# Kernel optimization log

Measured on AMD Instinct MI355X. Metric: run time of the kernel, lower is better.

Reference implementation:

```python
import jax, jax.numpy as jnp
import numpy as np

UP_RATIO = 2
DOWN_RATIO = 2
KS = 12  # up/down FIR kernel size
EPS = 1e-9


def kaiser_sinc_filter1d(cutoff, half_width, kernel_size):
    even = kernel_size % 2 == 0
    half_size = kernel_size // 2
    delta_f = 4.0 * half_width
    A = 2.285 * (half_size - 1) * np.pi * delta_f + 7.95
    if A > 50.0:
        beta = 0.1102 * (A - 8.7)
    elif A >= 21.0:
        beta = 0.5842 * (A - 21.0) ** 0.4 + 0.07886 * (A - 21.0)
    else:
        beta = 0.0
    window = np.kaiser(kernel_size, beta)
    if even:
        time = np.arange(-half_size, half_size) + 0.5
    else:
        time = np.arange(kernel_size) - half_size
    f = 2.0 * cutoff * window * np.sinc(2.0 * cutoff * time)
    f = f / f.sum()
    return f.astype(np.float32)


FILT_UP = jnp.asarray(kaiser_sinc_filter1d(0.5 / UP_RATIO, 0.6 / UP_RATIO, KS))
FILT_DOWN = jnp.asarray(kaiser_sinc_filter1d(0.5 / DOWN_RATIO, 0.6 / DOWN_RATIO, KS))


def _depthwise(x, w, strides, padding, lhs_dilation):
    # x: [B, C, T]; run depthwise FIR by folding channels into batch.
    B, C, T = x.shape
    y = jax.lax.conv_general_dilated(
        x.reshape(B * C, 1, T), w.reshape(1, 1, -1),
        window_strides=(strides,), padding=padding,
        lhs_dilation=(lhs_dilation,),
        dimension_numbers=("NCH", "OIH", "NCH"))
    return y.reshape(B, C, -1)


def upsample(x):
    # zero-stuff by ratio + symmetric kaiser-sinc FIR (== conv_transpose1d)
    k, r = KS, UP_RATIO
    pad = k // r - 1
    pad_left = pad * r + (k - r) // 2
    pad_right = pad * r + (k - r + 1) // 2
    x = jnp.pad(x, ((0, 0), (0, 0), (pad, pad)), mode="edge")
    y = r * _depthwise(x, FILT_UP, 1, [(k - 1, k - 1)], r)
    return y[..., pad_left:-pad_right]  # [B, C, 2T]


def downsample(x):
    k, r = KS, DOWN_RATIO
    pad_left = k // 2 - 1  # even kernel
    pad_right = k // 2
    x = jnp.pad(x, ((0, 0), (0, 0), (pad_left, pad_right)), mode="edge")
    return _depthwise(x, FILT_DOWN, r, "VALID", 1)  # [B, C, T]


def snake_beta(x, alpha_log, beta_log):
    # x + 1/(beta+eps) * sin(alpha*x)^2, alpha/beta = exp(log params), per channel
    a = jnp.exp(alpha_log)[None, :, None]
    b = jnp.exp(beta_log)[None, :, None]
    return x + (1.0 / (b + EPS)) * jnp.square(jnp.sin(a * x))


def alias_free_act(x, alpha_log, beta_log):
    return downsample(snake_beta(upsample(x), alpha_log, beta_log))


def conv1d(x, w, b, pad, dilation=1):
    y = jax.lax.conv_general_dilated(
        x, w, (1,), [(pad, pad)], rhs_dilation=(dilation,),
        dimension_numbers=("NCH", "OIH", "NCH"))
    return y + b[None, :, None]


def setup_inputs() -> dict:
    key = jax.random.key(0)
    ks = jax.random.split(key, 3)
    B, C, T = 8, 512, 8192
    x = jax.random.normal(ks[0], (B, C, T), dtype=jnp.float32)
    # init_weights: normal(0, 0.01)
    w1 = 0.01 * jax.random.normal(ks[1], (C, C, 3), dtype=jnp.float32)
    w2 = 0.01 * jax.random.normal(ks[2], (C, C, 3), dtype=jnp.float32)
    b1 = jnp.zeros((C,), dtype=jnp.float32)
    b2 = jnp.zeros((C,), dtype=jnp.float32)
    # SnakeBeta alpha_logscale=True: log-params init to zeros (alpha=beta=1)
    alpha1 = jnp.zeros((C,), dtype=jnp.float32)
    beta1 = jnp.zeros((C,), dtype=jnp.float32)
    alpha2 = jnp.zeros((C,), dtype=jnp.float32)
    beta2 = jnp.zeros((C,), dtype=jnp.float32)
    return {"x": x, "w1": w1, "b1": b1, "w2": w2, "b2": b2,
            "alpha1": alpha1, "beta1": beta1, "alpha2": alpha2, "beta2": beta2}


def reference(x, w1, b1, w2, b2, alpha1, beta1, alpha2, beta2):
    # AMPBlock0.forward: xt = a2(c2(a1(c1(a1(x))))); x = xt + x
    xt = alias_free_act(x, alpha1, beta1)
    xt = conv1d(xt, w1, b1, pad=1, dilation=1)  # dilation[0] == 1
    xt = alias_free_act(xt, alpha1, beta1)
    xt = conv1d(xt, w2, b2, pad=1, dilation=1)
    xt = alias_free_act(xt, alpha2, beta2)
    return xt + x
```

## Files before the change

kernel.cpp:

```cpp
#include <hip/hip_runtime.h>
#include <hip/hip_bf16.h>
#include <math.h>

#ifndef M_PI
#define M_PI 3.14159265358979323846
#endif

typedef __attribute__((ext_vector_type(8))) short bf16x8;
typedef __attribute__((ext_vector_type(4))) float f32x4;

struct Filt { float f[12]; };

static double bessel_i0(double x) {
  double sum = 1.0, term = 1.0;
  for (int k = 1; k < 64; ++k) {
    term *= x / (2.0 * k);
    double t2 = term * term;
    sum += t2;
    if (t2 < 1e-22 * sum) break;
  }
  return sum;
}

static void compute_filter(float* out12) {
  const int ks = 12;
  const double cutoff = 0.25, half_width = 0.3;
  const int half_size = 6;
  double delta_f = 4.0 * half_width;
  double A = 2.285 * (half_size - 1) * M_PI * delta_f + 7.95;
  double beta;
  if (A > 50.0)       beta = 0.1102 * (A - 8.7);
  else if (A >= 21.0) beta = 0.5842 * pow(A - 21.0, 0.4) + 0.07886 * (A - 21.0);
  else                beta = 0.0;
  double i0b = bessel_i0(beta);
  double f[12], s = 0.0;
  for (int n = 0; n < ks; ++n) {
    double ratio = (n - (ks - 1) / 2.0) / ((ks - 1) / 2.0);
    double arg = 1.0 - ratio * ratio;
    double wnd = bessel_i0(beta * sqrt(arg > 0.0 ? arg : 0.0)) / i0b;
    double time = (n - half_size) + 0.5;
    double xx = 2.0 * cutoff * time;
    double sinc = (xx == 0.0) ? 1.0 : sin(M_PI * xx) / (M_PI * xx);
    f[n] = 2.0 * cutoff * wnd * sinc;
    s += f[n];
  }
  for (int n = 0; n < ks; ++n) out12[n] = (float)(f[n] / s);
}

__device__ __forceinline__ ushort f2bf(float f) {
  __hip_bfloat16 h = __float2bfloat16(f);
  return *(ushort*)&h;
}

__device__ __forceinline__ void gl_lds16(const void* g, void* l) {
  __builtin_amdgcn_global_load_lds(
      (const __attribute__((address_space(1))) unsigned int*)g,
      (__attribute__((address_space(3))) unsigned int*)l, 16, 0, 0);
}

template <typename TIN, bool TOUT>
__global__ __launch_bounds__(512, 4) void act2(
    const TIN* __restrict__ in, void* __restrict__ out_,
    const float* __restrict__ alpha_log, const float* __restrict__ beta_log,
    const float* __restrict__ resid, int C, int T, Filt fl)
{
  __shared__ float xs[64 * 75];
  __shared__ float ys[TOUT ? 1 : 64 * 65];
  const int t0 = blockIdx.x * 64;
  const int c0 = blockIdx.y * 64;
  const int b  = blockIdx.z;
  const int tid = threadIdx.x;

  constexpr int NSTG = 64 * 74;
  float tmp[10];
#pragma unroll
  for (int k = 0; k < 10; ++k) {
    int i = tid + k * 512;
    if (i < NSTG) {
      int c = i / 74, j = i - c * 74;
      int t = min(max(t0 - 5 + j, 0), T - 1);
      tmp[k] = (float)in[((long)(b * C + c0 + c)) * T + t];
    }
  }
#pragma unroll
  for (int k = 0; k < 10; ++k) {
    int i = tid + k * 512;
    if (i < NSTG) {
      int c = i / 74, j = i - c * 74;
      xs[c * 75 + j] = tmp[k];
    }
  }
  __syncthreads();

  const int c  = tid & 63;
  const int tg = tid >> 6;
  const int tb = t0 + tg * 8;
  const float a  = __expf(alpha_log[c0 + c]);
  const float rb = 1.0f / (__expf(beta_log[c0 + c]) + 1e-9f);

  float sbv[26];
  const bool interior = (tb >= 8) && (tb <= T - 16);
  if (interior) {
    float xv[18];
    const float* xr = xs + c * 75 + tg * 8;
#pragma unroll
    for (int m = 0; m < 18; ++m) xv[m] = xr[m];
#pragma unroll
    for (int m = 0; m <= 12; ++m) {
      float uo = fl.f[1] * xv[m]     + fl.f[3] * xv[m + 1] + fl.f[5]  * xv[m + 2]
               + fl.f[7] * xv[m + 3] + fl.f[9] * xv[m + 4] + fl.f[11] * xv[m + 5];
      float ue = fl.f[0] * xv[m]     + fl.f[2] * xv[m + 1] + fl.f[4]  * xv[m + 2]
               + fl.f[6] * xv[m + 3] + fl.f[8] * xv[m + 4] + fl.f[10] * xv[m + 5];
      uo *= 2.0f; ue *= 2.0f;
      float s0 = __sinf(a * uo);
      float s1 = __sinf(a * ue);
      sbv[2 * m]     = uo + rb * s0 * s0;
      sbv[2 * m + 1] = ue + rb * s1 * s1;
    }
  } else {
    const float* xr = xs + c * 75;
#pragma unroll
    for (int j = 0; j < 26; ++j) {
      int p = 2 * tb - 5 + j;
      int pc = min(max(p, 0), 2 * T - 1);
      float up;
      if (pc & 1) {
        int q = (pc - 1) >> 1;
        int base = q - t0 + 3;
        up = fl.f[1] * xr[base]     + fl.f[3] * xr[base + 1] + fl.f[5]  * xr[base + 2]
           + fl.f[7] * xr[base + 3] + fl.f[9] * xr[base + 4] + fl.f[11] * xr[base + 5];
      } else {
        int q = pc >> 1;
        int base = q - t0 + 2;
        up = fl.f[0] * xr[base]     + fl.f[2] * xr[base + 1] + fl.f[4]  * xr[base + 2]
           + fl.f[6] * xr[base + 3] + fl.f[8] * xr[base + 4] + fl.f[10] * xr[base + 5];
      }
      up *= 2.0f;
      float s = __sinf(a * up);
      sbv[j] = up + rb * s * s;
    }
  }

  float acc[8];
#pragma unroll
  for (int i = 0; i < 8; ++i) {
    float s = 0.0f;
#pragma unroll
    for (int u = 0; u < 12; ++u) s += fl.f[u] * sbv[2 * i + u];
    acc[i] = s;
  }

  if constexpr (TOUT) {
    __hip_bfloat16* out = (__hip_bfloat16*)out_;
#pragma unroll
    for (int i = 0; i < 8; ++i)
      out[((long)b * T + tb + i) * C + c0 + c] = __float2bfloat16(acc[i]);
  } else {
    float* out = (float*)out_;
    const int cc0 = tid >> 4,        tq0 = (tid & 15) * 4;
    const int cc1 = cc0 + 32,        tq1 = tq0;
    const long o0 = ((long)(b * C + c0 + cc0)) * T + t0 + tq0;
    const long o1 = ((long)(b * C + c0 + cc1)) * T + t0 + tq1;
    const float4 r0 = *(const float4*)(resid + o0);
    const float4 r1 = *(const float4*)(resid + o1);
#pragma unroll
    for (int i = 0; i < 8; ++i) ys[c * 65 + tg * 8 + i] = acc[i];
    __syncthreads();
    float4 v0, v1;
    v0.x = ys[cc0 * 65 + tq0]     + r0.x;
    v0.y = ys[cc0 * 65 + tq0 + 1] + r0.y;
    v0.z = ys[cc0 * 65 + tq0 + 2] + r0.z;
    v0.w = ys[cc0 * 65 + tq0 + 3] + r0.w;
    v1.x = ys[cc1 * 65 + tq1]     + r1.x;
    v1.y = ys[cc1 * 65 + tq1 + 1] + r1.y;
    v1.z = ys[cc1 * 65 + tq1 + 2] + r1.z;
    v1.w = ys[cc1 * 65 + tq1 + 3] + r1.w;
    *(float4*)(out + o0) = v0;
    *(float4*)(out + o1) = v1;
  }
}

__global__ __launch_bounds__(256) void wconv(
    const float* __restrict__ w, ushort* __restrict__ wbf, int C)
{
  int idx = blockIdx.x * 256 + threadIdx.x;
  int total = 3 * C * C;
  if (idx >= total) return;
  int d = idx / (C * C);
  int r = idx - d * C * C;
  wbf[idx] = f2bf(w[(long)r * 3 + d]);
}

#define MT 64
#define NTC 256
#define BK 32

__global__ __launch_bounds__(256) void conv_mfma(
    const __hip_bfloat16* __restrict__ inT,
    const ushort* __restrict__ wbf,
    const float* __restrict__ bias,
    __hip_bfloat16* __restrict__ out,
    int C, int T)
{
  __shared__ ushort wl[3][MT][BK];
  __shared__ ushort xs[NTC + 2][BK];
  const int t0  = blockIdx.x * NTC;
  const int co0 = blockIdx.y * MT;
  const int b   = blockIdx.z;
  const int tid  = threadIdx.x;
  const int lane = tid & 63;
  const int wave = tid >> 6;
  const int ln15 = lane & 15;
  const int quad = lane >> 4;
  const ushort* inU = (const ushort*)inT;

  f32x4 acc[4][4];
#pragma unroll
  for (int mi = 0; mi < 4; ++mi)
#pragma unroll
    for (int ni = 0; ni < 4; ++ni) acc[mi][ni] = (f32x4){0.f, 0.f, 0.f, 0.f};

  ushort* wlf = &wl[0][0][0];
  ushort* xsf = &xs[0][0];

  for (int ci0 = 0; ci0 < C; ci0 += BK) {
    __syncthreads();
#pragma unroll
    for (int it = 0; it < 3; ++it) {
      int g = it * 256 + tid;
      int d = g >> 8, co = (g >> 2) & 63, seg = g & 3;
      const ushort* gsrc = wbf + ((long)d * C + co0 + co) * C + ci0 + seg * 8;
      gl_lds16(gsrc, wlf + (size_t)(it * 256 + (tid & ~63)) * 8);
    }
#pragma unroll
    for (int it = 0; it < 4; ++it) {
      int g = it * 256 + tid + 4;
      int tl = g >> 2, seg = g & 3;
      int t = t0 - 1 + tl;
      const ushort* gsrc = inU + ((long)b * T + t) * C + ci0 + seg * 8;
      gl_lds16(gsrc, xsf + (size_t)(it * 256 + (tid & ~63) + 4) * 8);
    }
    if (tid < 8) {
      int g = (tid < 4) ? tid : (1028 + tid - 4);
      int tl = g >> 2, seg = g & 3;
      int t = t0 - 1 + tl;
      uint4 v = {0u, 0u, 0u, 0u};
      if (t >= 0 && t < T)
        v = *(const uint4*)(inU + ((long)b * T + t) * C + ci0 + seg * 8);
      *(uint4*)&xs[tl][seg * 8] = v;
    }
    __syncthreads();

#pragma unroll
    for (int d = 0; d < 3; ++d) {
      bf16x8 afr[4], bfr[4];
#pragma unroll
      for (int mi = 0; mi < 4; ++mi)
        afr[mi] = *(const bf16x8*)&wl[d][mi * 16 + ln15][quad * 8];
#pragma unroll
      for (int ni = 0; ni < 4; ++ni)
        bfr[ni] = *(const bf16x8*)&xs[wave * 64 + ni * 16 + ln15 + d][quad * 8];
#pragma unroll
      for (int mi = 0; mi < 4; ++mi)
#pragma unroll
        for (int ni = 0; ni < 4; ++ni)
          acc[mi][ni] = __builtin_amdgcn_mfma_f32_16x16x32_bf16(
              afr[mi], bfr[ni], acc[mi][ni], 0, 0, 0);
    }
  }

#pragma unroll
  for (int mi = 0; mi < 4; ++mi) {
#pragma unroll
    for (int r = 0; r < 4; ++r) {
      int co = co0 + mi * 16 + quad * 4 + r;
      float bv = bias[co];
      long orow = ((long)(b * C + co)) * T;
#pragma unroll
      for (int ni = 0; ni < 4; ++ni) {
        int t = t0 + wave * 64 + ni * 16 + ln15;
        out[orow + t] = __float2bfloat16(acc[mi][ni][r] + bv);
      }
    }
  }
}

extern "C" void kernel_launch(void* const* d_in, const int* in_sizes, int n_in,
                              void* d_out, int out_size, void* d_ws, size_t ws_size,
                              hipStream_t stream) {
  const float* x      = (const float*)d_in[0];
  const float* w1     = (const float*)d_in[1];
  const float* b1     = (const float*)d_in[2];
  const float* w2     = (const float*)d_in[3];
  const float* b2     = (const float*)d_in[4];
  const float* alpha1 = (const float*)d_in[5];
  const float* beta1  = (const float*)d_in[6];
  const float* alpha2 = (const float*)d_in[7];
  const float* beta2  = (const float*)d_in[8];
  float* out = (float*)d_out;

  const int C = in_sizes[2];
  const long total = (long)in_sizes[0];
  const int T = 8192;
  const int B = (int)(total / ((long)C * T));

  __hip_bfloat16* ws0 = (__hip_bfloat16*)d_ws;
  __hip_bfloat16* ws1 = ws0 + (size_t)B * C * T;
  ushort* w1bf = (ushort*)d_out;
  ushort* w2bf = w1bf + (size_t)3 * C * C;

  Filt fl;
  compute_filter(fl.f);

  dim3 actGrid(T / 64, C / 64, B);
  dim3 convGrid(T / NTC, C / MT, B);
  int wblocks = (3 * C * C + 255) / 256;

  wconv<<<wblocks, 256, 0, stream>>>(w1, w1bf, C);
  wconv<<<wblocks, 256, 0, stream>>>(w2, w2bf, C);
  act2<float, true><<<actGrid, 512, 0, stream>>>(x, ws0, alpha1, beta1, nullptr, C, T, fl);
  conv_mfma<<<convGrid, 256, 0, stream>>>(ws0, w1bf, b1, ws1, C, T);
  act2<__hip_bfloat16, true><<<actGrid, 512, 0, stream>>>(ws1, ws0, alpha1, beta1, nullptr, C, T, fl);
  conv_mfma<<<convGrid, 256, 0, stream>>>(ws0, w2bf, b2, ws1, C, T);
  act2<__hip_bfloat16, false><<<actGrid, 512, 0, stream>>>(ws1, out, alpha2, beta2, x, C, T, fl);
}
```

Before: 892.2 us.

## Make act2 blocks loop over eight time tiles with register-prefetched inputs

Each activation block now walks eight consecutive 64-sample time tiles instead of one. While the current tile is being computed, the next tile's input is prefetched into registers, so global load latency can overlap with the sin/FIR arithmetic. The grid shrinks eightfold, which lowers parallelism per launch (B*C/64*16 blocks) and adds an extra barrier per tile plus higher register pressure from the double-buffered temporaries.

Measured after the change: 1.237 ms. +38.6%, slower.

```diff
diff --git a/kernel.cpp b/kernel.cpp
--- a/kernel.cpp
+++ b/kernel.cpp
@@ -58,6 +58,29 @@
       (__attribute__((address_space(3))) unsigned int*)l, 16, 0, 0);
 }
 
+#define NSTG (64 * 74)
+
+#define PREFETCH(T0, TMP)                                                \
+  _Pragma("unroll")                                                      \
+  for (int k = 0; k < 10; ++k) {                                         \
+    int i = tid + k * 512;                                               \
+    if (i < NSTG) {                                                      \
+      int cI = i / 74, jI = i - cI * 74;                                 \
+      int t = min(max((T0) - 5 + jI, 0), T - 1);                         \
+      TMP[k] = (float)in[((long)(b * C + c0 + cI)) * T + t];             \
+    }                                                                    \
+  }
+
+#define WRITE_XS(TMP)                                                    \
+  _Pragma("unroll")                                                      \
+  for (int k = 0; k < 10; ++k) {                                         \
+    int i = tid + k * 512;                                               \
+    if (i < NSTG) {                                                      \
+      int cI = i / 74, jI = i - cI * 74;                                 \
+      xs[cI * 75 + jI] = TMP[k];                                         \
+    }                                                                    \
+  }
+
 template <typename TIN, bool TOUT>
 __global__ __launch_bounds__(512, 4) void act2(
     const TIN* __restrict__ in, void* __restrict__ out_,
@@ -66,117 +89,112 @@
 {
   __shared__ float xs[64 * 75];
   __shared__ float ys[TOUT ? 1 : 64 * 65];
-  const int t0 = blockIdx.x * 64;
+  const int NT = 8;
+  const int tbase = blockIdx.x * (64 * NT);
   const int c0 = blockIdx.y * 64;
   const int b  = blockIdx.z;
   const int tid = threadIdx.x;
 
-  constexpr int NSTG = 64 * 74;
-  float tmp[10];
-#pragma unroll
-  for (int k = 0; k < 10; ++k) {
-    int i = tid + k * 512;
-    if (i < NSTG) {
-      int c = i / 74, j = i - c * 74;
-      int t = min(max(t0 - 5 + j, 0), T - 1);
-      tmp[k] = (float)in[((long)(b * C + c0 + c)) * T + t];
-    }
-  }
-#pragma unroll
-  for (int k = 0; k < 10; ++k) {
-    int i = tid + k * 512;
-    if (i < NSTG) {
-      int c = i / 74, j = i - c * 74;
-      xs[c * 75 + j] = tmp[k];
-    }
-  }
-  __syncthreads();
-
   const int c  = tid & 63;
   const int tg = tid >> 6;
-  const int tb = t0 + tg * 8;
   const float a  = __expf(alpha_log[c0 + c]);
   const float rb = 1.0f / (__expf(beta_log[c0 + c]) + 1e-9f);
 
-  float sbv[26];
-  const bool interior = (tb >= 8) && (tb <= T - 16);
-  if (interior) {
-    float xv[18];
-    const float* xr = xs + c * 75 + tg * 8;
-#pragma unroll
-    for (int m = 0; m < 18; ++m) xv[m] = xr[m];
-#pragma unroll
-    for (int m = 0; m <= 12; ++m) {
-      float uo = fl.f[1] * xv[m]     + fl.f[3] * xv[m + 1] + fl.f[5]  * xv[m + 2]
-               + fl.f[7] * xv[m + 3] + fl.f[9] * xv[m + 4] + fl.f[11] * xv[m + 5];
-      float ue = fl.f[0] * xv[m]     + fl.f[2] * xv[m + 1] + fl.f[4]  * xv[m + 2]
-               + fl.f[6] * xv[m + 3] + fl.f[8] * xv[m + 4] + fl.f[10] * xv[m + 5];
-      uo *= 2.0f; ue *= 2.0f;
-      float s0 = __sinf(a * uo);
-      float s1 = __sinf(a * ue);
-      sbv[2 * m]     = uo + rb * s0 * s0;
-      sbv[2 * m + 1] = ue + rb * s1 * s1;
-    }
-  } else {
-    const float* xr = xs + c * 75;
-#pragma unroll
-    for (int j = 0; j < 26; ++j) {
-      int p = 2 * tb - 5 + j;
-      int pc = min(max(p, 0), 2 * T - 1);
-      float up;
-      if (pc & 1) {
-        int q = (pc - 1) >> 1;
-        int base = q - t0 + 3;
-        up = fl.f[1] * xr[base]     + fl.f[3] * xr[base + 1] + fl.f[5]  * xr[base + 2]
-           + fl.f[7] * xr[base + 3] + fl.f[9] * xr[base + 4] + fl.f[11] * xr[base + 5];
-      } else {
-        int q = pc >> 1;
-        int base = q - t0 + 2;
-        up = fl.f[0] * xr[base]     + fl.f[2] * xr[base + 1] + fl.f[4]  * xr[base + 2]
-           + fl.f[6] * xr[base + 3] + fl.f[8] * xr[base + 4] + fl.f[10] * xr[base + 5];
+  float tmpA[10], tmpB[10];
+  PREFETCH(tbase, tmpA);
+
+  for (int tt = 0; tt < NT; ++tt) {
+    const int t0 = tbase + tt * 64;
+    WRITE_XS(tmpA);
+    __syncthreads();
+    if (tt + 1 < NT) { PREFETCH(t0 + 64, tmpB); }
+
+    const int tb = t0 + tg * 8;
+    float sbv[26];
+    const bool interior = (tb >= 8) && (tb <= T - 16);
+    if (interior) {
+      float xv[18];
+      const float* xr = xs + c * 75 + tg * 8;
+#pragma unroll
+      for (int m = 0; m < 18; ++m) xv[m] = xr[m];
+#pragma unroll
+      for (int m = 0; m <= 12; ++m) {
+        float uo = fl.f[1] * xv[m]     + fl.f[3] * xv[m + 1] + fl.f[5]  * xv[m + 2]
+                 + fl.f[7] * xv[m + 3] + fl.f[9] * xv[m + 4] + fl.f[11] * xv[m + 5];
+        float ue = fl.f[0] * xv[m]     + fl.f[2] * xv[m + 1] + fl.f[4]  * xv[m + 2]
+                 + fl.f[6] * xv[m + 3] + fl.f[8] * xv[m + 4] + fl.f[10] * xv[m + 5];
+        uo *= 2.0f; ue *= 2.0f;
+        float s0 = __sinf(a * uo);
+        float s1 = __sinf(a * ue);
+        sbv[2 * m]     = uo + rb * s0 * s0;
+        sbv[2 * m + 1] = ue + rb * s1 * s1;
       }
-      up *= 2.0f;
-      float s = __sinf(a * up);
-      sbv[j] = up + rb * s * s;
-    }
-  }
-
-  float acc[8];
-#pragma unroll
-  for (int i = 0; i < 8; ++i) {
-    float s = 0.0f;
-#pragma unroll
-    for (int u = 0; u < 12; ++u) s += fl.f[u] * sbv[2 * i + u];
-    acc[i] = s;
-  }
-
-  if constexpr (TOUT) {
-    __hip_bfloat16* out = (__hip_bfloat16*)out_;
-#pragma unroll
-    for (int i = 0; i < 8; ++i)
-      out[((long)b * T + tb + i) * C + c0 + c] = __float2bfloat16(acc[i]);
-  } else {
-    float* out = (float*)out_;
-    const int cc0 = tid >> 4,        tq0 = (tid & 15) * 4;
-    const int cc1 = cc0 + 32,        tq1 = tq0;
-    const long o0 = ((long)(b * C + c0 + cc0)) * T + t0 + tq0;
-    const long o1 = ((long)(b * C + c0 + cc1)) * T + t0 + tq1;
-    const float4 r0 = *(const float4*)(resid + o0);
-    const float4 r1 = *(const float4*)(resid + o1);
-#pragma unroll
-    for (int i = 0; i < 8; ++i) ys[c * 65 + tg * 8 + i] = acc[i];
-    __syncthreads();
-    float4 v0, v1;
-    v0.x = ys[cc0 * 65 + tq0]     + r0.x;
-    v0.y = ys[cc0 * 65 + tq0 + 1] + r0.y;
-    v0.z = ys[cc0 * 65 + tq0 + 2] + r0.z;
-    v0.w = ys[cc0 * 65 + tq0 + 3] + r0.w;
-    v1.x = ys[cc1 * 65 + tq1]     + r1.x;
-    v1.y = ys[cc1 * 65 + tq1 + 1] + r1.y;
-    v1.z = ys[cc1 * 65 + tq1 + 2] + r1.z;
-    v1.w = ys[cc1 * 65 + tq1 + 3] + r1.w;
-    *(float4*)(out + o0) = v0;
-    *(float4*)(out + o1) = v1;
+    } else {
+      const float* xr = xs + c * 75;
+#pragma unroll
+      for (int j = 0; j < 26; ++j) {
+        int p = 2 * tb - 5 + j;
+        int pc = min(max(p, 0), 2 * T - 1);
+        float up;
+        if (pc & 1) {
+          int q = (pc - 1) >> 1;
+          int base = q - t0 + 3;
+          up = fl.f[1] * xr[base]     + fl.f[3] * xr[base + 1] + fl.f[5]  * xr[base + 2]
+             + fl.f[7] * xr[base + 3] + fl.f[9] * xr[base + 4] + fl.f[11] * xr[base + 5];
+        } else {
+          int q = pc >> 1;
+          int base = q - t0 + 2;
+          up = fl.f[0] * xr[base]     + fl.f[2] * xr[base + 1] + fl.f[4]  * xr[base + 2]
+             + fl.f[6] * xr[base + 3] + fl.f[8] * xr[base + 4] + fl.f[10] * xr[base + 5];
+        }
+        up *= 2.0f;
+        float s = __sinf(a * up);
+        sbv[j] = up + rb * s * s;
+      }
+    }
+
+    float acc[8];
+#pragma unroll
+    for (int i = 0; i < 8; ++i) {
+      float s = 0.0f;
+#pragma unroll
+      for (int u = 0; u < 12; ++u) s += fl.f[u] * sbv[2 * i + u];
+      acc[i] = s;
+    }
+
+    if constexpr (TOUT) {
+      __hip_bfloat16* out = (__hip_bfloat16*)out_;
+#pragma unroll
+      for (int i = 0; i < 8; ++i)
+        out[((long)b * T + tb + i) * C + c0 + c] = __float2bfloat16(acc[i]);
+      __syncthreads();
+    } else {
+      float* out = (float*)out_;
+      const int cc0 = tid >> 4,   tq0 = (tid & 15) * 4;
+      const int cc1 = cc0 + 32,   tq1 = tq0;
+      const long o0 = ((long)(b * C + c0 + cc0)) * T + t0 + tq0;
+      const long o1 = ((long)(b * C + c0 + cc1)) * T + t0 + tq1;
+      const float4 r0 = *(const float4*)(resid + o0);
+      const float4 r1 = *(const float4*)(resid + o1);
+#pragma unroll
+      for (int i = 0; i < 8; ++i) ys[c * 65 + tg * 8 + i] = acc[i];
+      __syncthreads();
+      float4 v0, v1;
+      v0.x = ys[cc0 * 65 + tq0]     + r0.x;
+      v0.y = ys[cc0 * 65 + tq0 + 1] + r0.y;
+      v0.z = ys[cc0 * 65 + tq0 + 2] + r0.z;
+      v0.w = ys[cc0 * 65 + tq0 + 3] + r0.w;
+      v1.x = ys[cc1 * 65 + tq1]     + r1.x;
+      v1.y = ys[cc1 * 65 + tq1 + 1] + r1.y;
+      v1.z = ys[cc1 * 65 + tq1 + 2] + r1.z;
+      v1.w = ys[cc1 * 65 + tq1 + 3] + r1.w;
+      *(float4*)(out + o0) = v0;
+      *(float4*)(out + o1) = v1;
+      __syncthreads();
+    }
+
+#pragma unroll
+    for (int k = 0; k < 10; ++k) tmpA[k] = tmpB[k];
   }
 }
 
@@ -312,7 +330,7 @@
   Filt fl;
   compute_filter(fl.f);
 
-  dim3 actGrid(T / 64, C / 64, B);
+  dim3 actGrid(T / 512, C / 64, B);
   dim3 convGrid(T / NTC, C / MT, B);
   int wblocks = (3 * C * C + 255) / 256;
 
```

## Loop act2 over channel tiles with register-prefetched vectorized loads

Applied to the files above, without the earlier changes.

The activation kernel now gives each block all channels for one time tile and loops over 64-channel chunks. The next chunk's input is prefetched into registers with 16-byte vector loads while the current chunk is computed, replacing the earlier scalar strided loads. This is meant to hide global load latency and cut per-load instruction overhead. The cost is a grid that shrinks by a factor of C/64, which lowers parallelism, plus extra registers and barriers per iteration.

Result: faster. 770.0 us (-13.7%).

```diff
diff --git a/kernel.cpp b/kernel.cpp
--- a/kernel.cpp
+++ b/kernel.cpp
@@ -64,119 +64,189 @@
     const float* __restrict__ alpha_log, const float* __restrict__ beta_log,
     const float* __restrict__ resid, int C, int T, Filt fl)
 {
-  __shared__ float xs[64 * 75];
+  __shared__ float xs[64 * 81];
   __shared__ float ys[TOUT ? 1 : 64 * 65];
   const int t0 = blockIdx.x * 64;
-  const int c0 = blockIdx.y * 64;
   const int b  = blockIdx.z;
   const int tid = threadIdx.x;
-
-  constexpr int NSTG = 64 * 74;
-  float tmp[10];
-#pragma unroll
-  for (int k = 0; k < 10; ++k) {
-    int i = tid + k * 512;
-    if (i < NSTG) {
-      int c = i / 74, j = i - c * 74;
-      int t = min(max(t0 - 5 + j, 0), T - 1);
-      tmp[k] = (float)in[((long)(b * C + c0 + c)) * T + t];
-    }
-  }
-#pragma unroll
-  for (int k = 0; k < 10; ++k) {
-    int i = tid + k * 512;
-    if (i < NSTG) {
-      int c = i / 74, j = i - c * 74;
-      xs[c * 75 + j] = tmp[k];
-    }
-  }
-  __syncthreads();
-
   const int c  = tid & 63;
   const int tg = tid >> 6;
-  const int tb = t0 + tg * 8;
-  const float a  = __expf(alpha_log[c0 + c]);
-  const float rb = 1.0f / (__expf(beta_log[c0 + c]) + 1e-9f);
-
-  float sbv[26];
-  const bool interior = (tb >= 8) && (tb <= T - 16);
-  if (interior) {
-    float xv[18];
-    const float* xr = xs + c * 75 + tg * 8;
-#pragma unroll
-    for (int m = 0; m < 18; ++m) xv[m] = xr[m];
-#pragma unroll
-    for (int m = 0; m <= 12; ++m) {
-      float uo = fl.f[1] * xv[m]     + fl.f[3] * xv[m + 1] + fl.f[5]  * xv[m + 2]
-               + fl.f[7] * xv[m + 3] + fl.f[9] * xv[m + 4] + fl.f[11] * xv[m + 5];
-      float ue = fl.f[0] * xv[m]     + fl.f[2] * xv[m + 1] + fl.f[4]  * xv[m + 2]
-               + fl.f[6] * xv[m + 3] + fl.f[8] * xv[m + 4] + fl.f[10] * xv[m + 5];
-      uo *= 2.0f; ue *= 2.0f;
-      float s0 = __sinf(a * uo);
-      float s1 = __sinf(a * ue);
-      sbv[2 * m]     = uo + rb * s0 * s0;
-      sbv[2 * m + 1] = ue + rb * s1 * s1;
-    }
-  } else {
-    const float* xr = xs + c * 75;
-#pragma unroll
-    for (int j = 0; j < 26; ++j) {
-      int p = 2 * tb - 5 + j;
-      int pc = min(max(p, 0), 2 * T - 1);
-      float up;
-      if (pc & 1) {
-        int q = (pc - 1) >> 1;
-        int base = q - t0 + 3;
-        up = fl.f[1] * xr[base]     + fl.f[3] * xr[base + 1] + fl.f[5]  * xr[base + 2]
-           + fl.f[7] * xr[base + 3] + fl.f[9] * xr[base + 4] + fl.f[11] * xr[base + 5];
-      } else {
-        int q = pc >> 1;
-        int base = q - t0 + 2;
-        up = fl.f[0] * xr[base]     + fl.f[2] * xr[base + 1] + fl.f[4]  * xr[base + 2]
-           + fl.f[6] * xr[base + 3] + fl.f[8] * xr[base + 4] + fl.f[10] * xr[base + 5];
-      }
-      up *= 2.0f;
-      float s = __sinf(a * up);
-      sbv[j] = up + rb * s * s;
-    }
-  }
-
-  float acc[8];
-#pragma unroll
-  for (int i = 0; i < 8; ++i) {
-    float s = 0.0f;
-#pragma unroll
-    for (int u = 0; u < 12; ++u) s += fl.f[u] * sbv[2 * i + u];
-    acc[i] = s;
-  }
-
-  if constexpr (TOUT) {
-    __hip_bfloat16* out = (__hip_bfloat16*)out_;
-#pragma unroll
-    for (int i = 0; i < 8; ++i)
-      out[((long)b * T + tb + i) * C + c0 + c] = __float2bfloat16(acc[i]);
-  } else {
-    float* out = (float*)out_;
-    const int cc0 = tid >> 4,        tq0 = (tid & 15) * 4;
-    const int cc1 = cc0 + 32,        tq1 = tq0;
-    const long o0 = ((long)(b * C + c0 + cc0)) * T + t0 + tq0;
-    const long o1 = ((long)(b * C + c0 + cc1)) * T + t0 + tq1;
-    const float4 r0 = *(const float4*)(resid + o0);
-    const float4 r1 = *(const float4*)(resid + o1);
-#pragma unroll
-    for (int i = 0; i < 8; ++i) ys[c * 65 + tg * 8 + i] = acc[i];
+  const bool tEdge = (t0 < 8) || (t0 + 72 > T);
+  constexpr bool F32 = (sizeof(TIN) == 4);
+  constexpr int NREG = F32 ? 3 : 2;
+
+  float4 tA[NREG], tB[NREG];
+
+  auto prefetch = [&](int cb, float4* tt) {
+    if constexpr (F32) {
+#pragma unroll
+      for (int k = 0; k < 3; ++k) {
+        int i = tid + k * 512;
+        if (i < 1280) {
+          int cI = i / 20, jc = i - cI * 20;
+          const float* row = (const float*)in + (long)(b * C + cb + cI) * T;
+          if (!tEdge) {
+            tt[k] = *(const float4*)(row + t0 - 8 + 4 * jc);
+          } else {
+            float* e = (float*)&tt[k];
+#pragma unroll
+            for (int q = 0; q < 4; ++q) {
+              int t = min(max(t0 - 8 + 4 * jc + q, 0), T - 1);
+              e[q] = row[t];
+            }
+          }
+        }
+      }
+    } else {
+      const ushort* inU = (const ushort*)in;
+#pragma unroll
+      for (int k = 0; k < 2; ++k) {
+        int i = tid + k * 512;
+        if (i < 640) {
+          int cI = i / 10, jc = i - cI * 10;
+          const ushort* row = inU + (long)(b * C + cb + cI) * T;
+          if (!tEdge) {
+            tt[k] = *(const float4*)(row + t0 - 8 + 8 * jc);
+          } else {
+            ushort* e = (ushort*)&tt[k];
+#pragma unroll
+            for (int q = 0; q < 8; ++q) {
+              int t = min(max(t0 - 8 + 8 * jc + q, 0), T - 1);
+              e[q] = row[t];
+            }
+          }
+        }
+      }
+    }
+  };
+
+  auto writeXs = [&](const float4* tt) {
+    if constexpr (F32) {
+#pragma unroll
+      for (int k = 0; k < 3; ++k) {
+        int i = tid + k * 512;
+        if (i < 1280) {
+          int cI = i / 20, jc = i - cI * 20;
+          const float* e = (const float*)&tt[k];
+#pragma unroll
+          for (int q = 0; q < 4; ++q) xs[cI * 81 + 4 * jc + q] = e[q];
+        }
+      }
+    } else {
+#pragma unroll
+      for (int k = 0; k < 2; ++k) {
+        int i = tid + k * 512;
+        if (i < 640) {
+          int cI = i / 10, jc = i - cI * 10;
+          const ushort* e = (const ushort*)&tt[k];
+#pragma unroll
+          for (int q = 0; q < 8; ++q)
+            xs[cI * 81 + 8 * jc + q] = __uint_as_float((unsigned)e[q] << 16);
+        }
+      }
+    }
+  };
+
+  prefetch(0, tA);
+  float aRaw = alpha_log[c];
+  float bRaw = beta_log[c];
+
+  for (int cc = 0; cc < C; cc += 64) {
+    writeXs(tA);
     __syncthreads();
-    float4 v0, v1;
-    v0.x = ys[cc0 * 65 + tq0]     + r0.x;
-    v0.y = ys[cc0 * 65 + tq0 + 1] + r0.y;
-    v0.z = ys[cc0 * 65 + tq0 + 2] + r0.z;
-    v0.w = ys[cc0 * 65 + tq0 + 3] + r0.w;
-    v1.x = ys[cc1 * 65 + tq1]     + r1.x;
-    v1.y = ys[cc1 * 65 + tq1 + 1] + r1.y;
-    v1.z = ys[cc1 * 65 + tq1 + 2] + r1.z;
-    v1.w = ys[cc1 * 65 + tq1 + 3] + r1.w;
-    *(float4*)(out + o0) = v0;
-    *(float4*)(out + o1) = v1;
+    const bool more = (cc + 64 < C);
+    if (more) prefetch(cc + 64, tB);
+    const float a  = __expf(aRaw);
+    const float rb = 1.0f / (__expf(bRaw) + 1e-9f);
+    if (more) { aRaw = alpha_log[cc + 64 + c]; bRaw = beta_log[cc + 64 + c]; }
+
+    const int tb = t0 + tg * 8;
+    float sbv[26];
+    const bool interior = (tb >= 8) && (tb <= T - 16);
+    if (interior) {
+      float xv[18];
+      const float* xr = xs + c * 81 + tg * 8 + 3;
+#pragma unroll
+      for (int m = 0; m < 18; ++m) xv[m] = xr[m];
+#pragma unroll
+      for (int m = 0; m <= 12; ++m) {
+        float uo = fl.f[1] * xv[m]     + fl.f[3] * xv[m + 1] + fl.f[5]  * xv[m + 2]
+                 + fl.f[7] * xv[m + 3] + fl.f[9] * xv[m + 4] + fl.f[11] * xv[m + 5];
+        float ue = fl.f[0] * xv[m]     + fl.f[2] * xv[m + 1] + fl.f[4]  * xv[m + 2]
+                 + fl.f[6] * xv[m + 3] + fl.f[8] * xv[m + 4] + fl.f[10] * xv[m + 5];
+        uo *= 2.0f; ue *= 2.0f;
+        float s0 = __sinf(a * uo);
+        float s1 = __sinf(a * ue);
+        sbv[2 * m]     = uo + rb * s0 * s0;
+        sbv[2 * m + 1] = ue + rb * s1 * s1;
+      }
+    } else {
+      const float* xr = xs + c * 81;
+#pragma unroll
+      for (int j = 0; j < 26; ++j) {
+        int p = 2 * tb - 5 + j;
+        int pc = min(max(p, 0), 2 * T - 1);
+        float up;
+        if (pc & 1) {
+          int q = (pc - 1) >> 1;
+          int base = q - t0 + 6;
+          up = fl.f[1] * xr[base]     + fl.f[3] * xr[base + 1] + fl.f[5]  * xr[base + 2]
+             + fl.f[7] * xr[base + 3] + fl.f[9] * xr[base + 4] + fl.f[11] * xr[base + 5];
+        } else {
+          int q = pc >> 1;
+          int base = q - t0 + 5;
+          up = fl.f[0] * xr[base]     + fl.f[2] * xr[base + 1] + fl.f[4]  * xr[base + 2]
+             + fl.f[6] * xr[base + 3] + fl.f[8] * xr[base + 4] + fl.f[10] * xr[base + 5];
+        }
+        up *= 2.0f;
+        float s = __sinf(a * up);
+        sbv[j] = up + rb * s * s;
+      }
+    }
+
+    float acc[8];
+#pragma unroll
+    for (int i = 0; i < 8; ++i) {
+      float s = 0.0f;
+#pragma unroll
+      for (int u = 0; u < 12; ++u) s += fl.f[u] * sbv[2 * i + u];
+      acc[i] = s;
+    }
+
+    if constexpr (TOUT) {
+      __hip_bfloat16* out = (__hip_bfloat16*)out_;
+#pragma unroll
+      for (int i = 0; i < 8; ++i)
+        out[((long)b * T + tb + i) * C + cc + c] = __float2bfloat16(acc[i]);
+    } else {
+      float* out = (float*)out_;
+      const int rc0 = tid >> 4, tq = (tid & 15) * 4;
+      const int rc1 = rc0 + 32;
+      const long o0 = ((long)(b * C + cc + rc0)) * T + t0 + tq;
+      const long o1 = ((long)(b * C + cc + rc1)) * T + t0 + tq;
+      const float4 r0 = *(const float4*)(resid + o0);
+      const float4 r1 = *(const float4*)(resid + o1);
+#pragma unroll
+      for (int i = 0; i < 8; ++i) ys[c * 65 + tg * 8 + i] = acc[i];
+      __syncthreads();
+      float4 v0, v1;
+      v0.x = ys[rc0 * 65 + tq]     + r0.x;
+      v0.y = ys[rc0 * 65 + tq + 1] + r0.y;
+      v0.z = ys[rc0 * 65 + tq + 2] + r0.z;
+      v0.w = ys[rc0 * 65 + tq + 3] + r0.w;
+      v1.x = ys[rc1 * 65 + tq]     + r1.x;
+      v1.y = ys[rc1 * 65 + tq + 1] + r1.y;
+      v1.z = ys[rc1 * 65 + tq + 2] + r1.z;
+      v1.w = ys[rc1 * 65 + tq + 3] + r1.w;
+      *(float4*)(out + o0) = v0;
+      *(float4*)(out + o1) = v1;
+    }
+
+    __syncthreads();
+    if (more) {
+#pragma unroll
+      for (int k = 0; k < NREG; ++k) tA[k] = tB[k];
+    }
   }
 }
 
@@ -312,7 +382,7 @@
   Filt fl;
   compute_filter(fl.f);
 
-  dim3 actGrid(T / 64, C / 64, B);
+  dim3 actGrid(T / 64, 1, B);
   dim3 convGrid(T / NTC, C / MT, B);
   int wblocks = (3 * C * C + 255) / 256;
 
```
